# Performance work log

Measured on AMD Instinct MI355X. Metric: run time of the kernel, lower is better.

The kernel has to match this reference:

```python
import jax, jax.numpy as jnp
import numpy as np

BITS = 4
GROUP_SIZE = 128
MAXQ = (1 << BITS) - 1  # 15
PACK = 32 // BITS       # 8 nibbles per int32


def setup_inputs() -> dict:
    key = jax.random.key(0)
    k1, k2, k3, k4, k5 = jax.random.split(key, 5)
    infeatures, outfeatures, tokens = 8192, 8192, 4096
    n_groups = infeatures // GROUP_SIZE  # 64
    x = jax.random.normal(k1, (tokens, infeatures), dtype=jnp.float32)
    qweight = jax.random.randint(k2, (infeatures // PACK, outfeatures), 0, 2147483647, dtype=jnp.int32)
    qzeros = jax.random.randint(k3, (n_groups, outfeatures // PACK), 0, 2147483647, dtype=jnp.int32)
    scales = jax.random.uniform(k4, (n_groups, outfeatures), dtype=jnp.float32) * 0.01 + 0.001
    bias = jax.random.normal(k5, (outfeatures,), dtype=jnp.float32)
    return {"x": x, "qweight": qweight, "qzeros": qzeros, "scales": scales, "bias": bias}


def _dequant(qweight, qzeros, scales):
    shifts = jnp.arange(0, 32, BITS, dtype=jnp.int32)  # [8]
    # unpack weight nibbles: [in/8, 8, out] -> [n_groups, group_size, out]
    w = (qweight[:, None, :] >> shifts[None, :, None]) & MAXQ
    w = w.reshape(-1, GROUP_SIZE, qweight.shape[1])
    # unpack zero points: [ng, out/8, 8] -> [ng, out]; note stored as (zero-1)
    z = ((qzeros[:, :, None] >> shifts[None, None, :]) & MAXQ) + 1
    z = z.reshape(z.shape[0], -1)
    # groupwise dequant: scales * (w - z)
    W = scales[:, None, :] * (w.astype(scales.dtype) - z[:, None, :].astype(scales.dtype))
    return W.reshape(-1, W.shape[-1])  # [infeatures, outfeatures]


def reference(x, qweight, qzeros, scales, bias):
    W = _dequant(qweight, qzeros, scales)
    return x @ W + bias
```

## Files before the change

### kernel.cpp

```cpp
#include <hip/hip_runtime.h>
#include <hip/hip_bf16.h>

constexpr int MM = 4096;
constexpr int NN = 8192;
constexpr int KK = 8192;
constexpr int BM = 256, BN = 256, BK = 64;
constexpr int THREADS = 512;
constexpr int NKB = KK / BK;
constexpr int NT = NN / BN;
constexpr int NG = 64;

typedef _Float16 f16;
typedef __attribute__((ext_vector_type(2))) _Float16 f16x2;
typedef __attribute__((ext_vector_type(8))) _Float16 f16x8;
typedef __attribute__((ext_vector_type(4))) float floatx4;
typedef __attribute__((ext_vector_type(4))) int intx4;
typedef __bf16 bf16;
typedef __attribute__((ext_vector_type(8))) __bf16 bf16x8;

__device__ __forceinline__ void async_copy16(const void* g, void* l) {
    __builtin_amdgcn_global_load_lds(
        (const __attribute__((address_space(1))) void*)g,
        (__attribute__((address_space(3))) void*)l, 16, 0, 0);
}

__global__ __launch_bounds__(256)
void convert_x(const float* __restrict__ x, f16* __restrict__ xb) {
    const int base = blockIdx.x * 256 + threadIdx.x;
#pragma unroll
    for (int it = 0; it < 4; ++it) {
        const int tid = base + it * 1048576;
        const int c = tid & 7;
        const int m = (tid >> 3) & 255;
        const int kb = (tid >> 11) & 127;
        const int mtile = tid >> 18;
        const int row = mtile * 256 + m;
        const int col = kb * 64 + c * 8;
        const float4* src = (const float4*)(x + (size_t)row * KK + col);
        const float4 f0 = src[0];
        const float4 f1 = src[1];
        f16x8 v;
        v[0] = (f16)f0.x; v[1] = (f16)f1.x;
        v[2] = (f16)f0.y; v[3] = (f16)f1.y;
        v[4] = (f16)f0.z; v[5] = (f16)f1.z;
        v[6] = (f16)f0.w; v[7] = (f16)f1.w;
        const int dst_chunk = (tid & ~7) | (c ^ (m & 7));
        *(f16x8*)(xb + (size_t)dst_chunk * 8) = v;
    }
}

__global__ __launch_bounds__(256)
void prepack_b(const unsigned* __restrict__ qweight, unsigned* __restrict__ bpack) {
    const int C = blockIdx.x * 256 + threadIdx.x;
    const int q    = C & 3;
    const int lane = (C >> 2) & 63;
    const int wnh  = (C >> 8) & 1;
    const int kb   = (C >> 9) & 127;
    const int ntile = C >> 16;
    const int quad = lane >> 4, ml = lane & 15;
    const int ks = q >> 1, jh = q & 1;
    const int row = kb * 8 + ks * 4 + quad;
    const int colbase = ntile * 256 + wnh * 128 + ml + jh * 64;
    intx4 v;
#pragma unroll
    for (int j = 0; j < 4; ++j)
        v[j] = (int)qweight[(size_t)row * NN + colbase + j * 16];
    *(intx4*)(bpack + (size_t)C * 4) = v;
}

__global__ __launch_bounds__(256)
void prepack_s(const float* __restrict__ scales, const unsigned* __restrict__ qzeros,
               unsigned* __restrict__ spack) {
    const int T = blockIdx.x * 256 + threadIdx.x;
    const int lane = T & 63;
    const int wnh  = (T >> 6) & 1;
    const int g    = (T >> 7) & 63;
    const int ntile = T >> 13;
    const int ml = lane & 15;
    unsigned sp[8], nz[8];
#pragma unroll
    for (int jn = 0; jn < 8; ++jn) {
        const int col = ntile * 256 + wnh * 128 + ml + jn * 16;
        const float s = scales[(size_t)g * NN + col];
        const unsigned zw = qzeros[(size_t)g * (NN / 8) + (col >> 3)];
        const unsigned z = (zw >> (4 * (col & 7))) & 15u;
        const unsigned short sh = __builtin_bit_cast(unsigned short, (f16)s);
        sp[jn] = ((unsigned)sh << 16) | sh;
        const unsigned nh = 0xE401u + z;
        nz[jn] = (nh << 16) | nh;
    }
    unsigned* dst = spack + (size_t)T * 16;
    *(intx4*)(dst + 0)  = (intx4){(int)sp[0], (int)sp[1], (int)sp[2], (int)sp[3]};
    *(intx4*)(dst + 4)  = (intx4){(int)sp[4], (int)sp[5], (int)sp[6], (int)sp[7]};
    *(intx4*)(dst + 8)  = (intx4){(int)nz[0], (int)nz[1], (int)nz[2], (int)nz[3]};
    *(intx4*)(dst + 12) = (intx4){(int)nz[4], (int)nz[5], (int)nz[6], (int)nz[7]};
}

__global__ __launch_bounds__(THREADS, 2)
void qgemm(const f16* __restrict__ xb,
           const unsigned* __restrict__ bpack,
           const unsigned* __restrict__ spack,
           const float* __restrict__ bias,
           float* __restrict__ out)
{
    __shared__ alignas(16) f16 As[2][BM * BK];

    const int t = threadIdx.x;
    const int ntile = blockIdx.x & (NT - 1);
    const int mtile = blockIdx.x / NT;
    const int n0 = ntile * BN;

    const int wave = t >> 6;
    const int lane = t & 63;
    const int wm = (wave >> 1) * 64;
    const int wn = (wave & 1) * 128;
    const int ml = lane & 15;
    const int quad = lane >> 4;
    const int wnh = wave & 1;

    floatx4 acc[4][8];
#pragma unroll
    for (int i = 0; i < 4; ++i)
#pragma unroll
        for (int j = 0; j < 8; ++j)
            acc[i][j] = (floatx4){0.f, 0.f, 0.f, 0.f};

    unsigned bq[16];
    unsigned s_pk[8], nzp[8];

    const char* xb_base = (const char*)xb
        + (size_t)mtile * NKB * (BM * BK) * sizeof(f16);
    const unsigned bq_base0 = ((unsigned)(ntile * 128) * 2 + wnh) * 1024u + lane * 16u;
    const unsigned sp_base0 = ((unsigned)(ntile * 64) * 2 + wnh) * 1024u + lane * 16u;

    auto stage_a = [&](int kb, int buf) {
        const char* g = xb_base + (size_t)kb * (BM * BK * 2) + wave * 4096 + lane * 16;
        char* l = (char*)&As[buf][0] + wave * 4096;
#pragma unroll
        for (int i = 0; i < 4; ++i)
            async_copy16(g + i * 1024, l + i * 1024);
    };

    auto load_af = [&](int buf, int ks, f16x8 (&af)[4]) {
#pragma unroll
        for (int im = 0; im < 4; ++im) {
            const int r = wm + im * 16 + ml;
            const int clog = ks * 4 + quad;
            af[im] = *(const f16x8*)&As[buf][r * BK + ((clog ^ (r & 7)) << 3)];
        }
    };

    auto load_bq = [&](int kb, int q) {
        const unsigned idx = bq_base0 + (unsigned)kb * 2048u + (unsigned)q * 4u;
        *(intx4*)&bq[q * 4] = *(const intx4*)(bpack + idx);
    };

    auto load_grp = [&](int g) {
        const unsigned idx = sp_base0 + (unsigned)g * 2048u;
        *(intx4*)&s_pk[0] = *(const intx4*)(spack + idx);
        *(intx4*)&s_pk[4] = *(const intx4*)(spack + idx + 4);
        *(intx4*)&nzp[0]  = *(const intx4*)(spack + idx + 8);
        *(intx4*)&nzp[4]  = *(const intx4*)(spack + idx + 12);
    };

    auto phase = [&](int ks, int jh, const f16x8 (&af)[4]) {
        __builtin_amdgcn_s_setprio(1);
#pragma unroll
        for (int j = 0; j < 4; ++j) {
            const int jn = jh * 4 + j;
            const unsigned u = bq[(ks * 2 + jh) * 4 + j];
            const unsigned t0 = ( u         & 0x000F000Fu) | 0x64006400u;
            const unsigned t1 = ((u >> 4)   & 0x000F000Fu) | 0x64006400u;
            const unsigned t2 = ((u >> 8)   & 0x000F000Fu) | 0x64006400u;
            const unsigned t3 = ((u >> 12)  & 0x000F000Fu) | 0x64006400u;
            const f16x2 z2 = __builtin_bit_cast(f16x2, nzp[jn]);
            const f16x2 sp = __builtin_bit_cast(f16x2, s_pk[jn]);
            const f16x2 w0 = (__builtin_bit_cast(f16x2, t0) + z2) * sp;
            const f16x2 w1 = (__builtin_bit_cast(f16x2, t1) + z2) * sp;
            const f16x2 w2 = (__builtin_bit_cast(f16x2, t2) + z2) * sp;
            const f16x2 w3 = (__builtin_bit_cast(f16x2, t3) + z2) * sp;
            const intx4 bi = { __builtin_bit_cast(int, w0), __builtin_bit_cast(int, w1),
                               __builtin_bit_cast(int, w2), __builtin_bit_cast(int, w3) };
            const f16x8 bfr = __builtin_bit_cast(f16x8, bi);
#pragma unroll
            for (int im = 0; im < 4; ++im)
                acc[im][jn] = __builtin_amdgcn_mfma_f32_16x16x32_f16(
                    af[im], bfr, acc[im][jn], 0, 0, 0);
        }
        __builtin_amdgcn_s_setprio(0);
    };

    auto body = [&](int kb, int buf, bool stage, bool odd) {
        f16x8 af[4];
        if (stage) stage_a(kb + 1, buf ^ 1);
        load_af(buf, 0, af);
        phase(0, 0, af);
        if (stage) load_bq(kb + 1, 0);
        phase(0, 1, af);
        if (stage) load_bq(kb + 1, 1);
        load_af(buf, 1, af);
        phase(1, 0, af);
        if (stage) load_bq(kb + 1, 2);
        phase(1, 1, af);
        if (stage) load_bq(kb + 1, 3);
        if (stage && odd) load_grp((kb + 1) >> 1);
        if (stage) __syncthreads();
    };

    load_grp(0);
    stage_a(0, 0);
    load_bq(0, 0); load_bq(0, 1); load_bq(0, 2); load_bq(0, 3);
    __syncthreads();

    for (int kb = 0; kb < NKB - 2; kb += 2) {
        body(kb, 0, true, false);
        body(kb + 1, 1, true, true);
    }
    body(NKB - 2, 0, true, false);
    body(NKB - 1, 1, false, true);

#pragma unroll
    for (int jn = 0; jn < 8; ++jn) {
        const int ngl = n0 + wn + jn * 16 + ml;
        const float bv = bias[ngl];
#pragma unroll
        for (int im = 0; im < 4; ++im) {
            const int mg = mtile * BM + wm + im * 16 + quad * 4;
#pragma unroll
            for (int r = 0; r < 4; ++r)
                out[(size_t)(mg + r) * NN + ngl] = acc[im][jn][r] + bv;
        }
    }
}

__global__ __launch_bounds__(THREADS, 2)
void qgemm_fallback(const float* __restrict__ x,
                    const unsigned* __restrict__ qweight,
                    const unsigned* __restrict__ qzeros,
                    const float* __restrict__ scales,
                    const float* __restrict__ bias,
                    float* __restrict__ out)
{
    __shared__ bf16 As[BM * BK];
    __shared__ bf16 Bs[BN * BK];

    const int t = threadIdx.x;
    const int ntile = blockIdx.x & 31;
    const int mtile = blockIdx.x >> 5;
    const int m0 = mtile * BM;
    const int n0 = ntile * BN;
    const int wave = t >> 6;
    const int lane = t & 63;
    const int wm = (wave >> 1) * 64;
    const int wn = (wave & 1) * 128;
    const int ml = lane & 15;
    const int quad = lane >> 4;
    const int bn = t & 255;
    const int rbase = (t >> 8) * 4;
    const int gn = n0 + bn;

    floatx4 acc[4][8];
    for (int i = 0; i < 4; ++i)
        for (int j = 0; j < 8; ++j)
            acc[i][j] = (floatx4){0.f, 0.f, 0.f, 0.f};

    float s = 0.f, sz = 0.f;

    for (int kb = 0; kb < KK / BK; ++kb) {
        const int k0 = kb * BK;
        if ((kb & 1) == 0) {
            const int g = kb >> 1;
            s = scales[g * NN + gn];
            const unsigned zw = qzeros[g * (NN / 8) + (gn >> 3)];
            const float z = (float)(((zw >> (4 * (gn & 7))) & 15u) + 1u);
            sz = s * z;
        }
#pragma unroll
        for (int i = 0; i < 4; ++i) {
            const int chunk = t + THREADS * i;
            const int m = chunk >> 3;
            const int c = chunk & 7;
            const float4* src = (const float4*)(x + (size_t)(m0 + m) * KK + (k0 + c * 8));
            const float4 f0 = src[0];
            const float4 f1 = src[1];
            bf16x8 v;
            v[0] = (bf16)f0.x; v[1] = (bf16)f0.y; v[2] = (bf16)f0.z; v[3] = (bf16)f0.w;
            v[4] = (bf16)f1.x; v[5] = (bf16)f1.y; v[6] = (bf16)f1.z; v[7] = (bf16)f1.w;
            *(bf16x8*)&As[m * BK + ((c ^ (m & 7)) << 3)] = v;
        }
        const int kq0 = k0 >> 3;
#pragma unroll
        for (int i = 0; i < 4; ++i) {
            const int rq = rbase + i;
            const unsigned q = qweight[(size_t)(kq0 + rq) * NN + gn];
            bf16x8 v;
#pragma unroll
            for (int j = 0; j < 8; ++j) {
                const float f = (float)((q >> (4 * j)) & 15u) * s - sz;
                v[j] = (bf16)f;
            }
            *(bf16x8*)&Bs[bn * BK + ((rq ^ (bn & 7)) << 3)] = v;
        }
        __syncthreads();
#pragma unroll
        for (int ks = 0; ks < 2; ++ks) {
            const int clog = ks * 4 + quad;
            bf16x8 af[4];
            bf16x8 bfr[8];
#pragma unroll
            for (int im = 0; im < 4; ++im) {
                const int row = wm + im * 16 + ml;
                af[im] = *(const bf16x8*)&As[row * BK + ((clog ^ (row & 7)) << 3)];
            }
#pragma unroll
            for (int jn = 0; jn < 8; ++jn) {
                const int row = wn + jn * 16 + ml;
                bfr[jn] = *(const bf16x8*)&Bs[row * BK + ((clog ^ (row & 7)) << 3)];
            }
#pragma unroll
            for (int im = 0; im < 4; ++im)
#pragma unroll
                for (int jn = 0; jn < 8; ++jn)
                    acc[im][jn] = __builtin_amdgcn_mfma_f32_16x16x32_bf16(
                        af[im], bfr[jn], acc[im][jn], 0, 0, 0);
        }
        __syncthreads();
    }
#pragma unroll
    for (int jn = 0; jn < 8; ++jn) {
        const int ngl = n0 + wn + jn * 16 + ml;
        const float bv = bias[ngl];
#pragma unroll
        for (int im = 0; im < 4; ++im) {
            const int mg = m0 + wm + im * 16 + quad * 4;
#pragma unroll
            for (int r = 0; r < 4; ++r)
                out[(size_t)(mg + r) * NN + ngl] = acc[im][jn][r] + bv;
        }
    }
}

extern "C" void kernel_launch(void* const* d_in, const int* in_sizes, int n_in,
                              void* d_out, int out_size, void* d_ws, size_t ws_size,
                              hipStream_t stream) {
    const float*    x       = (const float*)d_in[0];
    const unsigned* qweight = (const unsigned*)d_in[1];
    const unsigned* qzeros  = (const unsigned*)d_in[2];
    const float*    scales  = (const float*)d_in[3];
    const float*    bias    = (const float*)d_in[4];
    float* out = (float*)d_out;

    const int grid = (MM / BM) * (NN / BN);

    const size_t xb_bytes = (size_t)MM * KK * sizeof(f16);
    const size_t bp_bytes = (size_t)(KK / 8) * NN * 4;
    const size_t sp_bytes = (size_t)32 * 64 * 2 * 64 * 16 * 4;

    if (ws_size >= xb_bytes + bp_bytes + sp_bytes) {
        f16*      xb    = (f16*)d_ws;
        unsigned* bpack = (unsigned*)((char*)d_ws + xb_bytes);
        unsigned* spack = (unsigned*)((char*)d_ws + xb_bytes + bp_bytes);
        convert_x<<<4096, 256, 0, stream>>>(x, xb);
        prepack_b<<<8192, 256, 0, stream>>>(qweight, bpack);
        prepack_s<<<1024, 256, 0, stream>>>(scales, qzeros, spack);
        qgemm<<<grid, THREADS, 0, stream>>>(xb, bpack, spack, bias, out);
    } else {
        qgemm_fallback<<<grid, THREADS, 0, stream>>>(x, qweight, qzeros, scales, bias, out);
    }
}
```

Measured before the change: 795.8 us.

## Shrink GEMM block tile to 128x256 with 4x2 wave layout and swizzled grid

```diff
diff --git a/kernel.cpp b/kernel.cpp
--- a/kernel.cpp
+++ b/kernel.cpp
@@ -4,11 +4,11 @@
 constexpr int MM = 4096;
 constexpr int NN = 8192;
 constexpr int KK = 8192;
-constexpr int BM = 256, BN = 256, BK = 64;
+constexpr int AM = 128, AN = 256, BK = 64;
 constexpr int THREADS = 512;
 constexpr int NKB = KK / BK;
-constexpr int NT = NN / BN;
-constexpr int NG = 64;
+constexpr int NTN = NN / AN;
+constexpr int NTM = MM / AM;
 
 typedef _Float16 f16;
 typedef __attribute__((ext_vector_type(2))) _Float16 f16x2;
@@ -31,10 +31,10 @@
     for (int it = 0; it < 4; ++it) {
         const int tid = base + it * 1048576;
         const int c = tid & 7;
-        const int m = (tid >> 3) & 255;
-        const int kb = (tid >> 11) & 127;
-        const int mtile = tid >> 18;
-        const int row = mtile * 256 + m;
+        const int m = (tid >> 3) & 127;
+        const int kb = (tid >> 10) & 127;
+        const int mtile = tid >> 17;
+        const int row = mtile * AM + m;
         const int col = kb * 64 + c * 8;
         const float4* src = (const float4*)(x + (size_t)row * KK + col);
         const float4 f0 = src[0];
@@ -52,15 +52,14 @@
 __global__ __launch_bounds__(256)
 void prepack_b(const unsigned* __restrict__ qweight, unsigned* __restrict__ bpack) {
     const int C = blockIdx.x * 256 + threadIdx.x;
-    const int q    = C & 3;
-    const int lane = (C >> 2) & 63;
-    const int wnh  = (C >> 8) & 1;
+    const int ks   = C & 1;
+    const int lane = (C >> 1) & 63;
+    const int wq   = (C >> 7) & 3;
     const int kb   = (C >> 9) & 127;
     const int ntile = C >> 16;
     const int quad = lane >> 4, ml = lane & 15;
-    const int ks = q >> 1, jh = q & 1;
     const int row = kb * 8 + ks * 4 + quad;
-    const int colbase = ntile * 256 + wnh * 128 + ml + jh * 64;
+    const int colbase = ntile * 256 + wq * 64 + ml;
     intx4 v;
 #pragma unroll
     for (int j = 0; j < 4; ++j)
@@ -73,14 +72,14 @@
                unsigned* __restrict__ spack) {
     const int T = blockIdx.x * 256 + threadIdx.x;
     const int lane = T & 63;
-    const int wnh  = (T >> 6) & 1;
-    const int g    = (T >> 7) & 63;
-    const int ntile = T >> 13;
+    const int wq   = (T >> 6) & 3;
+    const int g    = (T >> 8) & 63;
+    const int ntile = T >> 14;
     const int ml = lane & 15;
-    unsigned sp[8], nz[8];
-#pragma unroll
-    for (int jn = 0; jn < 8; ++jn) {
-        const int col = ntile * 256 + wnh * 128 + ml + jn * 16;
+    unsigned sp[4], nz[4];
+#pragma unroll
+    for (int jn = 0; jn < 4; ++jn) {
+        const int col = ntile * 256 + wq * 64 + ml + jn * 16;
         const float s = scales[(size_t)g * NN + col];
         const unsigned zw = qzeros[(size_t)g * (NN / 8) + (col >> 3)];
         const unsigned z = (zw >> (4 * (col & 7))) & 15u;
@@ -89,55 +88,55 @@
         const unsigned nh = 0xE401u + z;
         nz[jn] = (nh << 16) | nh;
     }
-    unsigned* dst = spack + (size_t)T * 16;
-    *(intx4*)(dst + 0)  = (intx4){(int)sp[0], (int)sp[1], (int)sp[2], (int)sp[3]};
-    *(intx4*)(dst + 4)  = (intx4){(int)sp[4], (int)sp[5], (int)sp[6], (int)sp[7]};
-    *(intx4*)(dst + 8)  = (intx4){(int)nz[0], (int)nz[1], (int)nz[2], (int)nz[3]};
-    *(intx4*)(dst + 12) = (intx4){(int)nz[4], (int)nz[5], (int)nz[6], (int)nz[7]};
-}
-
-__global__ __launch_bounds__(THREADS, 2)
+    unsigned* dst = spack + (size_t)T * 8;
+    *(intx4*)(dst + 0) = (intx4){(int)sp[0], (int)sp[1], (int)sp[2], (int)sp[3]};
+    *(intx4*)(dst + 4) = (intx4){(int)nz[0], (int)nz[1], (int)nz[2], (int)nz[3]};
+}
+
+__global__ __launch_bounds__(THREADS, 4)
 void qgemm(const f16* __restrict__ xb,
            const unsigned* __restrict__ bpack,
            const unsigned* __restrict__ spack,
            const float* __restrict__ bias,
            float* __restrict__ out)
 {
-    __shared__ alignas(16) f16 As[2][BM * BK];
+    __shared__ alignas(16) f16 As[2][AM * BK];
 
     const int t = threadIdx.x;
-    const int ntile = blockIdx.x & (NT - 1);
-    const int mtile = blockIdx.x / NT;
-    const int n0 = ntile * BN;
+    const int v = (blockIdx.x & 7) * 128 + (blockIdx.x >> 3);
+    const int ntile = v & (NTN - 1);
+    const int mtile = v >> 5;
+    const int n0 = ntile * AN;
 
     const int wave = t >> 6;
     const int lane = t & 63;
-    const int wm = (wave >> 1) * 64;
-    const int wn = (wave & 1) * 128;
+    const int wm = (wave >> 2) * 64;
+    const int wn = (wave & 3) * 64;
     const int ml = lane & 15;
     const int quad = lane >> 4;
-    const int wnh = wave & 1;
-
-    floatx4 acc[4][8];
+    const int wq = wave & 3;
+
+    floatx4 acc[4][4];
 #pragma unroll
     for (int i = 0; i < 4; ++i)
 #pragma unroll
-        for (int j = 0; j < 8; ++j)
+        for (int j = 0; j < 4; ++j)
             acc[i][j] = (floatx4){0.f, 0.f, 0.f, 0.f};
 
-    unsigned bq[16];
-    unsigned s_pk[8], nzp[8];
+    unsigned bq[8];
+    unsigned s_pk[4], nzp[4];
 
     const char* xb_base = (const char*)xb
-        + (size_t)mtile * NKB * (BM * BK) * sizeof(f16);
-    const unsigned bq_base0 = ((unsigned)(ntile * 128) * 2 + wnh) * 1024u + lane * 16u;
-    const unsigned sp_base0 = ((unsigned)(ntile * 64) * 2 + wnh) * 1024u + lane * 16u;
+        + (size_t)mtile * NKB * (AM * BK) * sizeof(f16);
+    const unsigned bq_base0 = (unsigned)ntile * 262144u + (unsigned)wq * 512u + lane * 8u;
+    const unsigned sp_base0 = (unsigned)ntile * 131072u + (unsigned)wq * 512u + lane * 8u;
 
     auto stage_a = [&](int kb, int buf) {
-        const char* g = xb_base + (size_t)kb * (BM * BK * 2) + wave * 4096 + lane * 16;
-        char* l = (char*)&As[buf][0] + wave * 4096;
-#pragma unroll
-        for (int i = 0; i < 4; ++i)
+        const char* g = xb_base + (size_t)kb * (AM * BK * 2)
+                      + wave * 2048 + lane * 16;
+        char* l = (char*)&As[buf][0] + wave * 2048;
+#pragma unroll
+        for (int i = 0; i < 2; ++i)
             async_copy16(g + i * 1024, l + i * 1024);
     };
 
@@ -150,31 +149,28 @@
         }
     };
 
-    auto load_bq = [&](int kb, int q) {
-        const unsigned idx = bq_base0 + (unsigned)kb * 2048u + (unsigned)q * 4u;
-        *(intx4*)&bq[q * 4] = *(const intx4*)(bpack + idx);
+    auto load_bq = [&](int kb, int ks) {
+        const unsigned idx = bq_base0 + (unsigned)kb * 2048u + (unsigned)ks * 4u;
+        *(intx4*)&bq[ks * 4] = *(const intx4*)(bpack + idx);
     };
 
     auto load_grp = [&](int g) {
         const unsigned idx = sp_base0 + (unsigned)g * 2048u;
         *(intx4*)&s_pk[0] = *(const intx4*)(spack + idx);
-        *(intx4*)&s_pk[4] = *(const intx4*)(spack + idx + 4);
-        *(intx4*)&nzp[0]  = *(const intx4*)(spack + idx + 8);
-        *(intx4*)&nzp[4]  = *(const intx4*)(spack + idx + 12);
-    };
-
-    auto phase = [&](int ks, int jh, const f16x8 (&af)[4]) {
+        *(intx4*)&nzp[0]  = *(const intx4*)(spack + idx + 4);
+    };
+
+    auto phase = [&](int ks, const f16x8 (&af)[4]) {
         __builtin_amdgcn_s_setprio(1);
 #pragma unroll
         for (int j = 0; j < 4; ++j) {
-            const int jn = jh * 4 + j;
-            const unsigned u = bq[(ks * 2 + jh) * 4 + j];
+            const unsigned u = bq[ks * 4 + j];
             const unsigned t0 = ( u         & 0x000F000Fu) | 0x64006400u;
             const unsigned t1 = ((u >> 4)   & 0x000F000Fu) | 0x64006400u;
             const unsigned t2 = ((u >> 8)   & 0x000F000Fu) | 0x64006400u;
             const unsigned t3 = ((u >> 12)  & 0x000F000Fu) | 0x64006400u;
-            const f16x2 z2 = __builtin_bit_cast(f16x2, nzp[jn]);
-            const f16x2 sp = __builtin_bit_cast(f16x2, s_pk[jn]);
+            const f16x2 z2 = __builtin_bit_cast(f16x2, nzp[j]);
+            const f16x2 sp = __builtin_bit_cast(f16x2, s_pk[j]);
             const f16x2 w0 = (__builtin_bit_cast(f16x2, t0) + z2) * sp;
             const f16x2 w1 = (__builtin_bit_cast(f16x2, t1) + z2) * sp;
             const f16x2 w2 = (__builtin_bit_cast(f16x2, t2) + z2) * sp;
@@ -184,8 +180,8 @@
             const f16x8 bfr = __builtin_bit_cast(f16x8, bi);
 #pragma unroll
             for (int im = 0; im < 4; ++im)
-                acc[im][jn] = __builtin_amdgcn_mfma_f32_16x16x32_f16(
-                    af[im], bfr, acc[im][jn], 0, 0, 0);
+                acc[im][j] = __builtin_amdgcn_mfma_f32_16x16x32_f16(
+                    af[im], bfr, acc[im][j], 0, 0, 0);
         }
         __builtin_amdgcn_s_setprio(0);
     };
@@ -194,22 +190,18 @@
         f16x8 af[4];
         if (stage) stage_a(kb + 1, buf ^ 1);
         load_af(buf, 0, af);
-        phase(0, 0, af);
+        phase(0, af);
         if (stage) load_bq(kb + 1, 0);
-        phase(0, 1, af);
+        load_af(buf, 1, af);
+        phase(1, af);
         if (stage) load_bq(kb + 1, 1);
-        load_af(buf, 1, af);
-        phase(1, 0, af);
-        if (stage) load_bq(kb + 1, 2);
-        phase(1, 1, af);
-        if (stage) load_bq(kb + 1, 3);
         if (stage && odd) load_grp((kb + 1) >> 1);
         if (stage) __syncthreads();
     };
 
     load_grp(0);
     stage_a(0, 0);
-    load_bq(0, 0); load_bq(0, 1); load_bq(0, 2); load_bq(0, 3);
+    load_bq(0, 0); load_bq(0, 1);
     __syncthreads();
 
     for (int kb = 0; kb < NKB - 2; kb += 2) {
@@ -220,12 +212,12 @@
     body(NKB - 1, 1, false, true);
 
 #pragma unroll
-    for (int jn = 0; jn < 8; ++jn) {
+    for (int jn = 0; jn < 4; ++jn) {
         const int ngl = n0 + wn + jn * 16 + ml;
         const float bv = bias[ngl];
 #pragma unroll
         for (int im = 0; im < 4; ++im) {
-            const int mg = mtile * BM + wm + im * 16 + quad * 4;
+            const int mg = mtile * AM + wm + im * 16 + quad * 4;
 #pragma unroll
             for (int r = 0; r < 4; ++r)
                 out[(size_t)(mg + r) * NN + ngl] = acc[im][jn][r] + bv;
@@ -233,7 +225,7 @@
     }
 }
 
-__global__ __launch_bounds__(THREADS, 2)
+__global__ __launch_bounds__(512, 2)
 void qgemm_fallback(const float* __restrict__ x,
                     const unsigned* __restrict__ qweight,
                     const unsigned* __restrict__ qzeros,
@@ -241,14 +233,15 @@
                     const float* __restrict__ bias,
                     float* __restrict__ out)
 {
-    __shared__ bf16 As[BM * BK];
-    __shared__ bf16 Bs[BN * BK];
+    constexpr int FBM = 256, FBN = 256;
+    __shared__ bf16 As[FBM * BK];
+    __shared__ bf16 Bs[FBN * BK];
 
     const int t = threadIdx.x;
     const int ntile = blockIdx.x & 31;
     const int mtile = blockIdx.x >> 5;
-    const int m0 = mtile * BM;
-    const int n0 = ntile * BN;
+    const int m0 = mtile * FBM;
+    const int n0 = ntile * FBN;
     const int wave = t >> 6;
     const int lane = t & 63;
     const int wm = (wave >> 1) * 64;
@@ -277,7 +270,7 @@
         }
 #pragma unroll
         for (int i = 0; i < 4; ++i) {
-            const int chunk = t + THREADS * i;
+            const int chunk = t + 512 * i;
             const int m = chunk >> 3;
             const int c = chunk & 7;
             const float4* src = (const float4*)(x + (size_t)(m0 + m) * KK + (k0 + c * 8));
@@ -350,11 +343,9 @@
     const float*    bias    = (const float*)d_in[4];
     float* out = (float*)d_out;
 
-    const int grid = (MM / BM) * (NN / BN);
-
     const size_t xb_bytes = (size_t)MM * KK * sizeof(f16);
     const size_t bp_bytes = (size_t)(KK / 8) * NN * 4;
-    const size_t sp_bytes = (size_t)32 * 64 * 2 * 64 * 16 * 4;
+    const size_t sp_bytes = (size_t)32 * 64 * 4 * 64 * 8 * 4;
 
     if (ws_size >= xb_bytes + bp_bytes + sp_bytes) {
         f16*      xb    = (f16*)d_ws;
@@ -362,9 +353,11 @@
         unsigned* spack = (unsigned*)((char*)d_ws + xb_bytes + bp_bytes);
         convert_x<<<4096, 256, 0, stream>>>(x, xb);
         prepack_b<<<8192, 256, 0, stream>>>(qweight, bpack);
-        prepack_s<<<1024, 256, 0, stream>>>(scales, qzeros, spack);
+        prepack_s<<<2048, 256, 0, stream>>>(scales, qzeros, spack);
+        const int grid = NTM * NTN;
         qgemm<<<grid, THREADS, 0, stream>>>(xb, bpack, spack, bias, out);
     } else {
-        qgemm_fallback<<<grid, THREADS, 0, stream>>>(x, qweight, qzeros, scales, bias, out);
-    }
-}
+        const int grid = (MM / 256) * (NN / 256);
+        qgemm_fallback<<<grid, 512, 0, stream>>>(x, qweight, qzeros, scales, bias, out);
+    }
+}
```

Result: faster. 778.9 us (-2.1%).
